# Optimization experiments

Measured on AMD Instinct MI355X. Metric: run time of the kernel, lower is better.

The kernel has to match this reference:

```python
import jax, jax.numpy as jnp
import numpy as np

D_MODEL = 1024
N_HEAD = 16
HEAD_DIM = D_MODEL // N_HEAD
B, S = 4, 2048


def setup_inputs() -> dict:
    key = jax.random.key(0)
    ks = jax.random.split(key, 11)
    s = 1.0 / np.sqrt(D_MODEL)
    return {
        "query": jax.random.normal(ks[0], (B, S, D_MODEL), jnp.float32),
        "key": jax.random.normal(ks[1], (B, S, D_MODEL), jnp.float32),
        "value": jax.random.normal(ks[2], (B, S, D_MODEL), jnp.float32),
        "Wq": jax.random.normal(ks[3], (D_MODEL, D_MODEL), jnp.float32) * s,
        "bq": jax.random.normal(ks[4], (D_MODEL,), jnp.float32) * s,
        "Wk": jax.random.normal(ks[5], (D_MODEL, D_MODEL), jnp.float32) * s,
        "bk": jax.random.normal(ks[6], (D_MODEL,), jnp.float32) * s,
        "Wv": jax.random.normal(ks[7], (D_MODEL, D_MODEL), jnp.float32) * s,
        "bv": jax.random.normal(ks[8], (D_MODEL,), jnp.float32) * s,
        "Wo": jax.random.normal(ks[9], (D_MODEL, D_MODEL), jnp.float32) * s,
        "bo": jax.random.normal(ks[10], (D_MODEL,), jnp.float32) * s,
    }


def reference(query, key, value, Wq, bq, Wk, bk, Wv, bv, Wo, bo):
    b, s, d_model = query.shape
    # projections; reshape to [b, h, s, hd]
    def proj(x, W, bias):
        return (x @ W + bias).reshape(b, s, N_HEAD, HEAD_DIM).transpose(0, 2, 1, 3)
    q = proj(query, Wq, bq)
    k = proj(key, Wk, bk)
    v = proj(value, Wv, bv)
    # NOTE: original code scales by sqrt(d_model) (bug-faithful), not sqrt(head_dim)
    scores = jnp.einsum("bhqd,bhkd->bhqk", q, k) / jnp.sqrt(jnp.float32(d_model))
    causal = jnp.tril(jnp.ones((s, s), dtype=bool))
    scores = jnp.where(causal[None, None], scores, -jnp.inf)
    p = jax.nn.softmax(scores, axis=-1)  # dropout is identity in eval
    x = jnp.einsum("bhqk,bhkd->bhqd", p, v)
    x = x.transpose(0, 2, 1, 3).reshape(b, s, d_model)
    return x @ Wo + bo
```

## Files before the change

### kernel.cpp

```cpp
#include <hip/hip_runtime.h>
#include <hip/hip_bf16.h>
#include <cstdint>
#include <cstddef>

#define D_MODEL 1024
#define N_HEAD 16
#define HEAD_DIM 64
#define BATCH 4
#define SEQ 2048
#define M_ROWS (BATCH * SEQ)

typedef __attribute__((ext_vector_type(8))) short short8v;
typedef __attribute__((ext_vector_type(4))) float f32x4;
typedef __attribute__((ext_vector_type(16))) float f32x16;

__device__ __forceinline__ unsigned short f2bf(float f) {
    union { uint32_t i; float f; } c;
    c.f = f;
    uint32_t r = c.i + 0x7FFFu + ((c.i >> 16) & 1u);
    return (unsigned short)(r >> 16);
}
__device__ __forceinline__ unsigned short trunc_bf(float f) {
    return (unsigned short)(__float_as_uint(f) >> 16);
}
__device__ __forceinline__ uint32_t pack_trunc2(float a, float b) {
    return __builtin_amdgcn_perm(__float_as_uint(b), __float_as_uint(a), 0x07060302u);
}
__device__ __forceinline__ uint32_t pack_rne2(float a, float b) {
    return (uint32_t)f2bf(a) | ((uint32_t)f2bf(b) << 16);
}

struct __align__(16) U4 { uint32_t x, y, z, w; };
struct __align__(8) U2 { uint32_t x, y; };

__device__ __forceinline__ int sw_off(int row, int gl) {
    return row * 64 + ((gl ^ (row & 7)) << 3);
}

__device__ __forceinline__ void gload16(const unsigned short *g, unsigned short *l) {
    __builtin_amdgcn_global_load_lds((const __attribute__((address_space(1))) void *)g,
                                     (__attribute__((address_space(3))) void *)l, 16, 0, 0);
}

__global__ __launch_bounds__(256)
void cvt_kernel(const float *__restrict__ src, unsigned short *__restrict__ dst)
{
    const size_t i = ((size_t)blockIdx.x * 256 + threadIdx.x) * 8;
    float4 lo = *(const float4 *)(src + i);
    float4 hi = *(const float4 *)(src + i + 4);
    U4 pk;
    pk.x = pack_trunc2(lo.x, lo.y);
    pk.y = pack_trunc2(lo.z, lo.w);
    pk.z = pack_trunc2(hi.x, hi.y);
    pk.w = pack_trunc2(hi.z, hi.w);
    *(U4 *)(dst + i) = pk;
}

__global__ __launch_bounds__(256)
void wtrans_kernel(const float *__restrict__ W, unsigned short *__restrict__ Wt)
{
    __shared__ float tile[32][33];
    const int t = threadIdx.x;
    const int tx = t & 31, ty = t >> 5;
    const int bk = blockIdx.y * 32, bn = blockIdx.x * 32;
#pragma unroll
    for (int i = 0; i < 4; i++)
        tile[ty + 8 * i][tx] = W[(size_t)(bk + ty + 8 * i) * D_MODEL + bn + tx];
    __syncthreads();
#pragma unroll
    for (int i = 0; i < 4; i++)
        Wt[(size_t)(bn + ty + 8 * i) * D_MODEL + bk + tx] = trunc_bf(tile[tx][ty + 8 * i]);
}

template <typename TA, int MODE, typename TO>
__global__ __launch_bounds__(256, 2)
void mgemm_kernel(const TA *__restrict__ A,
                  const unsigned short *__restrict__ Wt,
                  const float *__restrict__ bias,
                  TO *__restrict__ out,
                  float escale)
{
    __shared__ __align__(16) unsigned short At[2][128 * 64];
    __shared__ __align__(16) unsigned short Bt[2][128 * 64];

    const int t = threadIdx.x;
    const int wave = t >> 6;
    const int lane = t & 63;
    const int n_ = lane & 15;
    const int quad = lane >> 4;
    const int wm = wave >> 1, wn = wave & 1;
    const int m0 = blockIdx.x * 128;
    const int n0 = blockIdx.y * 128;

    f32x4 acc[4][4];
#pragma unroll
    for (int i = 0; i < 4; i++)
#pragma unroll
        for (int j = 0; j < 4; j++) acc[i][j] = (f32x4){0.f, 0.f, 0.f, 0.f};

    const int srow = t >> 3;
    const int sg = t & 7;
    const int rl = lane >> 3;
    const int gsw = (lane & 7) ^ rl;

    for (int k0 = 0; k0 < D_MODEL; k0 += 128) {
        __syncthreads();
        if constexpr (sizeof(TA) == 2) {
            const unsigned short *Ab = (const unsigned short *)A;
#pragma unroll
            for (int h = 0; h < 2; h++)
#pragma unroll
                for (int c = 0; c < 4; c++) {
                    const int rb = wave * 32 + c * 8;
                    gload16(Ab + (size_t)(m0 + rb + rl) * D_MODEL + k0 + h * 64 + (gsw << 3),
                            &At[h][rb * 64]);
                    gload16(Wt + (size_t)(n0 + rb + rl) * D_MODEL + k0 + h * 64 + (gsw << 3),
                            &Bt[h][rb * 64]);
                }
        } else {
#pragma unroll
            for (int h = 0; h < 2; h++) {
#pragma unroll
                for (int i = 0; i < 4; i++) {
                    const int r = srow + 32 * i;
                    const float *p =
                        (const float *)A + (size_t)(m0 + r) * D_MODEL + k0 + h * 64 + sg * 8;
                    float4 lo = *(const float4 *)p;
                    float4 hi = *(const float4 *)(p + 4);
                    U4 pk;
                    pk.x = pack_trunc2(lo.x, lo.y);
                    pk.y = pack_trunc2(lo.z, lo.w);
                    pk.z = pack_trunc2(hi.x, hi.y);
                    pk.w = pack_trunc2(hi.z, hi.w);
                    *(U4 *)&At[h][sw_off(r, sg)] = pk;
                }
#pragma unroll
                for (int i = 0; i < 4; i++) {
                    const int r = srow + 32 * i;
                    const unsigned short *p =
                        Wt + (size_t)(n0 + r) * D_MODEL + k0 + h * 64 + sg * 8;
                    *(U4 *)&Bt[h][sw_off(r, sg)] = *(const U4 *)p;
                }
            }
        }
        __syncthreads();

#pragma unroll
        for (int c = 0; c < 4; c++) {
            const int bk_ = c >> 1, cc = c & 1;
            short8v af[4], bf[4];
#pragma unroll
            for (int mt = 0; mt < 4; mt++)
                af[mt] = *(const short8v *)&At[bk_][sw_off(wm * 64 + mt * 16 + n_, cc * 4 + quad)];
#pragma unroll
            for (int nt = 0; nt < 4; nt++)
                bf[nt] = *(const short8v *)&Bt[bk_][sw_off(wn * 64 + nt * 16 + n_, cc * 4 + quad)];
#pragma unroll
            for (int mt = 0; mt < 4; mt++)
#pragma unroll
                for (int nt = 0; nt < 4; nt++)
                    acc[mt][nt] = __builtin_amdgcn_mfma_f32_16x16x32_bf16(
                        af[mt], bf[nt], acc[mt][nt], 0, 0, 0);
        }
    }

    float bi[4];
#pragma unroll
    for (int nt = 0; nt < 4; nt++) bi[nt] = bias[n0 + wn * 64 + nt * 16 + n_];

    if constexpr (MODE == 2) {
#pragma unroll
        for (int mt = 0; mt < 4; mt++) {
            const int m = m0 + wm * 64 + mt * 16 + quad * 4;
#pragma unroll
            for (int nt = 0; nt < 4; nt++) {
                const int col = n0 + wn * 64 + nt * 16 + n_;
                const size_t idx = ((size_t)(m >> 11) * D_MODEL + col) * SEQ + (m & 2047);
                U2 pk;
                pk.x = pack_rne2(acc[mt][nt][0] + bi[nt], acc[mt][nt][1] + bi[nt]);
                pk.y = pack_rne2(acc[mt][nt][2] + bi[nt], acc[mt][nt][3] + bi[nt]);
                *(U2 *)((unsigned short *)out + idx) = pk;
            }
        }
    } else {
#pragma unroll
        for (int mt = 0; mt < 4; mt++)
#pragma unroll
            for (int reg = 0; reg < 4; reg++) {
                const int m = m0 + wm * 64 + mt * 16 + quad * 4 + reg;
#pragma unroll
                for (int nt = 0; nt < 4; nt++) {
                    const int col = n0 + wn * 64 + nt * 16 + n_;
                    const float v = (acc[mt][nt][reg] + bi[nt]) * escale;
                    if constexpr (MODE == 1)
                        ((unsigned short *)out)[(size_t)m * D_MODEL + col] = f2bf(v);
                    else
                        ((float *)out)[(size_t)m * D_MODEL + col] = v;
                }
            }
    }
}

__global__ __launch_bounds__(256, 2)
void attn_kernel(const unsigned short *Qg,
                 const unsigned short *__restrict__ Kg,
                 const unsigned short *__restrict__ VTg,
                 unsigned short *AO)
{
    __shared__ __align__(16) unsigned short Kt[64 * 64];
    __shared__ __align__(16) unsigned short Vt[64 * 64];

    const int h = blockIdx.x;
    const int b = blockIdx.y;
    const int qpair = blockIdx.z;
    const int t = threadIdx.x;
    const int w = t >> 6;
    const int lane = t & 63;
    const int ql = lane & 31;
    const int hi = lane >> 5;

    const size_t row_base = (size_t)b * SEQ * D_MODEL + h * HEAD_DIM;
    const size_t vhead = (size_t)(b * N_HEAD + h) * HEAD_DIM * SEQ;

    const int r0 = t >> 3;
    const int g = t & 7;

#pragma unroll
    for (int pass = 0; pass < 2; ++pass) {
        const int qb = pass ? (15 - qpair) : qpair;
        const int qs0 = qb * 128 + w * 32;
        const int qseq = qs0 + ql;

        short8v qf[4];
#pragma unroll
        for (int c = 0; c < 4; c++)
            qf[c] = *(const short8v *)(Qg + row_base + (size_t)qseq * D_MODEL + c * 16 + hi * 8);

        float m_i = -INFINITY, l_i = 0.f;
        f32x16 Oacc[2];
#pragma unroll
        for (int dt = 0; dt < 2; dt++)
#pragma unroll
            for (int i = 0; i < 16; i++) Oacc[dt][i] = 0.f;

        const int kb_max = 2 * qb + 1;

        for (int kb = 0; kb <= kb_max; ++kb) {
            __syncthreads();
#pragma unroll
            for (int i = 0; i < 2; i++) {
                const int r = r0 + 32 * i;
                U4 kv = *(const U4 *)(Kg + row_base + (size_t)(kb * 64 + r) * D_MODEL + g * 8);
                *(U4 *)&Kt[sw_off(r, g)] = kv;
                U4 vv = *(const U4 *)(VTg + vhead + (size_t)r * SEQ + kb * 64 + g * 8);
                *(U4 *)&Vt[sw_off(r, g)] = vv;
            }
            __syncthreads();

            if (kb * 64 > qs0 + 31) continue;

            f32x16 st[2];
            __builtin_amdgcn_s_setprio(1);
#pragma unroll
            for (int kt = 0; kt < 2; kt++) {
#pragma unroll
                for (int i = 0; i < 16; i++) st[kt][i] = 0.f;
#pragma unroll
                for (int c = 0; c < 4; c++) {
                    short8v kf = *(const short8v *)&Kt[sw_off(kt * 32 + ql, c * 2 + hi)];
                    st[kt] = __builtin_amdgcn_mfma_f32_32x32x16_bf16(kf, qf[c], st[kt], 0, 0, 0);
                }
            }
            __builtin_amdgcn_s_setprio(0);

            if (kb * 64 + 63 > qs0) {
#pragma unroll
                for (int kt = 0; kt < 2; kt++)
#pragma unroll
                    for (int r = 0; r < 16; r++) {
                        const int kseq = kb * 64 + kt * 32 + (r & 3) + 8 * (r >> 2) + 4 * hi;
                        if (kseq > qseq) st[kt][r] = -INFINITY;
                    }
            }

            float mx = -INFINITY;
#pragma unroll
            for (int kt = 0; kt < 2; kt++)
#pragma unroll
                for (int r = 0; r < 16; r++) mx = fmaxf(mx, st[kt][r]);
            mx = fmaxf(mx, __shfl_xor(mx, 32, 64));
            const float mnew = fmaxf(m_i, mx);
            const float alpha = __builtin_amdgcn_exp2f(m_i - mnew);
            m_i = mnew;
            float rs = 0.f;
#pragma unroll
            for (int kt = 0; kt < 2; kt++)
#pragma unroll
                for (int r = 0; r < 16; r++) {
                    const float p = __builtin_amdgcn_exp2f(st[kt][r] - mnew);
                    st[kt][r] = p;
                    rs += p;
                }
            rs += __shfl_xor(rs, 32, 64);
            l_i = l_i * alpha + rs;
#pragma unroll
            for (int dt = 0; dt < 2; dt++)
#pragma unroll
                for (int r = 0; r < 16; r++) Oacc[dt][r] *= alpha;

            short8v pf[4];
#pragma unroll
            for (int tt = 0; tt < 4; tt++) {
                const int kt = tt >> 1, o = (tt & 1) * 8;
                const uint32_t A  = pack_trunc2(st[kt][o + 0], st[kt][o + 1]);
                const uint32_t A2 = pack_trunc2(st[kt][o + 2], st[kt][o + 3]);
                const uint32_t B  = pack_trunc2(st[kt][o + 4], st[kt][o + 5]);
                const uint32_t B2 = pack_trunc2(st[kt][o + 6], st[kt][o + 7]);
                const uint32_t c1 = (uint32_t)__shfl_xor((int)(hi ? A : B), 32, 64);
                const uint32_t c2 = (uint32_t)__shfl_xor((int)(hi ? A2 : B2), 32, 64);
                union { uint32_t u[4]; short8v s; } cv;
                cv.u[0] = hi ? c1 : A;
                cv.u[1] = hi ? c2 : A2;
                cv.u[2] = hi ? B : c1;
                cv.u[3] = hi ? B2 : c2;
                pf[tt] = cv.s;
            }

            __builtin_amdgcn_s_setprio(1);
#pragma unroll
            for (int dt = 0; dt < 2; dt++)
#pragma unroll
                for (int tt = 0; tt < 4; tt++) {
                    short8v vf = *(const short8v *)&Vt[sw_off(dt * 32 + ql, tt * 2 + hi)];
                    Oacc[dt] = __builtin_amdgcn_mfma_f32_32x32x16_bf16(vf, pf[tt], Oacc[dt], 0, 0, 0);
                }
            __builtin_amdgcn_s_setprio(0);
        }

        const float linv = 1.f / l_i;
        const size_t obase = row_base + (size_t)qseq * D_MODEL;
#pragma unroll
        for (int dt = 0; dt < 2; dt++)
#pragma unroll
            for (int rg = 0; rg < 4; rg++) {
                const int d0 = dt * 32 + 8 * rg + 4 * hi;
                U2 pk;
                pk.x = (uint32_t)f2bf(Oacc[dt][4 * rg + 0] * linv) |
                       ((uint32_t)f2bf(Oacc[dt][4 * rg + 1] * linv) << 16);
                pk.y = (uint32_t)f2bf(Oacc[dt][4 * rg + 2] * linv) |
                       ((uint32_t)f2bf(Oacc[dt][4 * rg + 3] * linv) << 16);
                *(U2 *)(AO + obase + d0) = pk;
            }
    }
}

extern "C" void kernel_launch(void *const *d_in, const int *in_sizes, int n_in,
                              void *d_out, int out_size, void *d_ws, size_t ws_size,
                              hipStream_t stream)
{
    const float *q  = (const float *)d_in[0];
    const float *k  = (const float *)d_in[1];
    const float *v  = (const float *)d_in[2];
    const float *Wq = (const float *)d_in[3];
    const float *bq = (const float *)d_in[4];
    const float *Wk = (const float *)d_in[5];
    const float *bk = (const float *)d_in[6];
    const float *Wv = (const float *)d_in[7];
    const float *bv = (const float *)d_in[8];
    const float *Wo = (const float *)d_in[9];
    const float *bo = (const float *)d_in[10];
    float *out = (float *)d_out;

    const size_t TENS = (size_t)M_ROWS * D_MODEL;
    const size_t WT = (size_t)D_MODEL * D_MODEL;

    unsigned short *qbuf = (unsigned short *)d_ws;
    unsigned short *kbuf = qbuf + TENS;
    unsigned short *vtbuf = kbuf + TENS;
    unsigned short *cbuf = vtbuf + TENS;
    unsigned short *wt_new = cbuf + TENS;
    unsigned short *wt_old = vtbuf + TENS;

    dim3 wgrid(32, 32);
    dim3 ggrid(M_ROWS / 128, D_MODEL / 128);
    const int cgrid = (int)(TENS / 8 / 256);

    const float qscale = 0.03125f * 1.44269504088896341f;

    const size_t need_new = (5 * TENS + WT) * sizeof(unsigned short);

    if (ws_size >= need_new) {
        unsigned short *wt = wt_new;
        wtrans_kernel<<<wgrid, 256, 0, stream>>>(Wq, wt);
        cvt_kernel<<<cgrid, 256, 0, stream>>>(q, cbuf);
        mgemm_kernel<unsigned short, 1, unsigned short><<<ggrid, 256, 0, stream>>>(cbuf, wt, bq, qbuf, qscale);
        wtrans_kernel<<<wgrid, 256, 0, stream>>>(Wk, wt);
        cvt_kernel<<<cgrid, 256, 0, stream>>>(k, cbuf);
        mgemm_kernel<unsigned short, 1, unsigned short><<<ggrid, 256, 0, stream>>>(cbuf, wt, bk, kbuf, 1.f);
        wtrans_kernel<<<wgrid, 256, 0, stream>>>(Wv, wt);
        cvt_kernel<<<cgrid, 256, 0, stream>>>(v, cbuf);
        mgemm_kernel<unsigned short, 2, unsigned short><<<ggrid, 256, 0, stream>>>(cbuf, wt, bv, vtbuf, 1.f);

        attn_kernel<<<dim3(N_HEAD, BATCH, SEQ / 256), 256, 0, stream>>>(qbuf, kbuf, vtbuf, qbuf);

        wtrans_kernel<<<wgrid, 256, 0, stream>>>(Wo, wt);
        mgemm_kernel<unsigned short, 3, float><<<ggrid, 256, 0, stream>>>(qbuf, wt, bo, out, 1.f);
    } else {
        unsigned short *wt = wt_old;
        wtrans_kernel<<<wgrid, 256, 0, stream>>>(Wq, wt);
        mgemm_kernel<float, 1, unsigned short><<<ggrid, 256, 0, stream>>>(q, wt, bq, qbuf, qscale);
        wtrans_kernel<<<wgrid, 256, 0, stream>>>(Wk, wt);
        mgemm_kernel<float, 1, unsigned short><<<ggrid, 256, 0, stream>>>(k, wt, bk, kbuf, 1.f);
        wtrans_kernel<<<wgrid, 256, 0, stream>>>(Wv, wt);
        mgemm_kernel<float, 2, unsigned short><<<ggrid, 256, 0, stream>>>(v, wt, bv, vtbuf, 1.f);

        attn_kernel<<<dim3(N_HEAD, BATCH, SEQ / 256), 256, 0, stream>>>(qbuf, kbuf, vtbuf, qbuf);

        wtrans_kernel<<<wgrid, 256, 0, stream>>>(Wo, wt);
        mgemm_kernel<unsigned short, 3, float><<<ggrid, 256, 0, stream>>>(qbuf, wt, bo, out, 1.f);
    }
}
```

Measured before the change: 321.4 us.

## Batch Q/K projections in one GEMM launch and stage 128-key blocks in attention

Adds a combined Q/K projection GEMM that runs both projections in a single launch via a z-grid dimension. It uses single-buffered LDS at higher occupancy and reuses the output buffer as scratch for converted K. The attention kernel now loads two 64-key K/V tiles per sync step, which halves the number of barrier round-trips. The trade-off is double the LDS in attention and a new GEMM variant with no double buffering, which may expose load latency.

After: 321.9 us. No clear change (+0.2%).

```diff
diff --git a/kernel.cpp b/kernel.cpp
--- a/kernel.cpp
+++ b/kernel.cpp
@@ -72,6 +72,86 @@
         Wt[(size_t)(bn + ty + 8 * i) * D_MODEL + bk + tx] = trunc_bf(tile[tx][ty + 8 * i]);
 }
 
+__global__ __launch_bounds__(256, 4)
+void qk_gemm_kernel(const unsigned short *__restrict__ cq,
+                    const unsigned short *__restrict__ ckb,
+                    const unsigned short *__restrict__ wt2,
+                    const float *__restrict__ bq, const float *__restrict__ bk,
+                    unsigned short *__restrict__ oq, unsigned short *__restrict__ ok,
+                    float qscale)
+{
+    __shared__ __align__(16) unsigned short At[128 * 64];
+    __shared__ __align__(16) unsigned short Bt[128 * 64];
+
+    const int z = blockIdx.z;
+    const unsigned short *A = z ? ckb : cq;
+    const unsigned short *Wt = wt2 + (size_t)z * D_MODEL * D_MODEL;
+    const float *bias = z ? bk : bq;
+    unsigned short *out = z ? ok : oq;
+    const float es = z ? 1.f : qscale;
+
+    const int t = threadIdx.x;
+    const int wave = t >> 6;
+    const int lane = t & 63;
+    const int n_ = lane & 15;
+    const int quad = lane >> 4;
+    const int wm = wave >> 1, wn = wave & 1;
+    const int m0 = blockIdx.x * 128;
+    const int n0 = blockIdx.y * 128;
+
+    f32x4 acc[4][4];
+#pragma unroll
+    for (int i = 0; i < 4; i++)
+#pragma unroll
+        for (int j = 0; j < 4; j++) acc[i][j] = (f32x4){0.f, 0.f, 0.f, 0.f};
+
+    const int rl = lane >> 3;
+    const int gsw = (lane & 7) ^ rl;
+
+    for (int k0 = 0; k0 < D_MODEL; k0 += 64) {
+        __syncthreads();
+#pragma unroll
+        for (int c = 0; c < 4; c++) {
+            const int rb = wave * 32 + c * 8;
+            gload16(A + (size_t)(m0 + rb + rl) * D_MODEL + k0 + (gsw << 3), &At[rb * 64]);
+            gload16(Wt + (size_t)(n0 + rb + rl) * D_MODEL + k0 + (gsw << 3), &Bt[rb * 64]);
+        }
+        __syncthreads();
+
+#pragma unroll
+        for (int c = 0; c < 2; c++) {
+            short8v af[4], bf[4];
+#pragma unroll
+            for (int mt = 0; mt < 4; mt++)
+                af[mt] = *(const short8v *)&At[sw_off(wm * 64 + mt * 16 + n_, c * 4 + quad)];
+#pragma unroll
+            for (int nt = 0; nt < 4; nt++)
+                bf[nt] = *(const short8v *)&Bt[sw_off(wn * 64 + nt * 16 + n_, c * 4 + quad)];
+#pragma unroll
+            for (int mt = 0; mt < 4; mt++)
+#pragma unroll
+                for (int nt = 0; nt < 4; nt++)
+                    acc[mt][nt] = __builtin_amdgcn_mfma_f32_16x16x32_bf16(
+                        af[mt], bf[nt], acc[mt][nt], 0, 0, 0);
+        }
+    }
+
+    float bi[4];
+#pragma unroll
+    for (int nt = 0; nt < 4; nt++) bi[nt] = bias[n0 + wn * 64 + nt * 16 + n_];
+#pragma unroll
+    for (int mt = 0; mt < 4; mt++)
+#pragma unroll
+        for (int reg = 0; reg < 4; reg++) {
+            const int m = m0 + wm * 64 + mt * 16 + quad * 4 + reg;
+#pragma unroll
+            for (int nt = 0; nt < 4; nt++) {
+                const int col = n0 + wn * 64 + nt * 16 + n_;
+                out[(size_t)m * D_MODEL + col] = f2bf((acc[mt][nt][reg] + bi[nt]) * es);
+            }
+        }
+}
+
 template <typename TA, int MODE, typename TO>
 __global__ __launch_bounds__(256, 2)
 void mgemm_kernel(const TA *__restrict__ A,
@@ -207,8 +287,8 @@
                  const unsigned short *__restrict__ VTg,
                  unsigned short *AO)
 {
-    __shared__ __align__(16) unsigned short Kt[64 * 64];
-    __shared__ __align__(16) unsigned short Vt[64 * 64];
+    __shared__ __align__(16) unsigned short Kt[2][64 * 64];
+    __shared__ __align__(16) unsigned short Vt[2][64 * 64];
 
     const int h = blockIdx.x;
     const int b = blockIdx.y;
@@ -243,98 +323,106 @@
 #pragma unroll
             for (int i = 0; i < 16; i++) Oacc[dt][i] = 0.f;
 
-        const int kb_max = 2 * qb + 1;
-
-        for (int kb = 0; kb <= kb_max; ++kb) {
+        const int nst = qb + 1;
+
+        for (int s = 0; s <= nst - 1; ++s) {
             __syncthreads();
 #pragma unroll
-            for (int i = 0; i < 2; i++) {
-                const int r = r0 + 32 * i;
-                U4 kv = *(const U4 *)(Kg + row_base + (size_t)(kb * 64 + r) * D_MODEL + g * 8);
-                *(U4 *)&Kt[sw_off(r, g)] = kv;
-                U4 vv = *(const U4 *)(VTg + vhead + (size_t)r * SEQ + kb * 64 + g * 8);
-                *(U4 *)&Vt[sw_off(r, g)] = vv;
+            for (int bk2 = 0; bk2 < 2; bk2++)
+#pragma unroll
+                for (int i = 0; i < 2; i++) {
+                    const int r = r0 + 32 * i;
+                    U4 kv = *(const U4 *)(Kg + row_base +
+                                          (size_t)(s * 128 + bk2 * 64 + r) * D_MODEL + g * 8);
+                    *(U4 *)&Kt[bk2][sw_off(r, g)] = kv;
+                    U4 vv = *(const U4 *)(VTg + vhead + (size_t)r * SEQ + s * 128 + bk2 * 64 + g * 8);
+                    *(U4 *)&Vt[bk2][sw_off(r, g)] = vv;
+                }
+            __syncthreads();
+
+#pragma unroll
+            for (int h2 = 0; h2 < 2; h2++) {
+                const int kv0 = s * 128 + h2 * 64;
+                if (kv0 > qs0 + 31) continue;
+
+                f32x16 st[2];
+                __builtin_amdgcn_s_setprio(1);
+#pragma unroll
+                for (int kt = 0; kt < 2; kt++) {
+#pragma unroll
+                    for (int i = 0; i < 16; i++) st[kt][i] = 0.f;
+#pragma unroll
+                    for (int c = 0; c < 4; c++) {
+                        short8v kf = *(const short8v *)&Kt[h2][sw_off(kt * 32 + ql, c * 2 + hi)];
+                        st[kt] = __builtin_amdgcn_mfma_f32_32x32x16_bf16(kf, qf[c], st[kt], 0, 0, 0);
+                    }
+                }
+                __builtin_amdgcn_s_setprio(0);
+
+                if (kv0 + 63 > qs0) {
+#pragma unroll
+                    for (int kt = 0; kt < 2; kt++)
+#pragma unroll
+                        for (int r = 0; r < 16; r++) {
+                            const int kseq = kv0 + kt * 32 + (r & 3) + 8 * (r >> 2) + 4 * hi;
+                            if (kseq > qseq) st[kt][r] = -INFINITY;
+                        }
+                }
+
+                float mx = -INFINITY;
+#pragma unroll
+                for (int kt = 0; kt < 2; kt++)
+#pragma unroll
+                    for (int r = 0; r < 16; r++) mx = fmaxf(mx, st[kt][r]);
+                mx = fmaxf(mx, __shfl_xor(mx, 32, 64));
+                const float mnew = fmaxf(m_i, mx);
+                const float alpha = __builtin_amdgcn_exp2f(m_i - mnew);
+                m_i = mnew;
+                float rs = 0.f;
+#pragma unroll
+                for (int kt = 0; kt < 2; kt++)
+#pragma unroll
+                    for (int r = 0; r < 16; r++) {
+                        const float p = __builtin_amdgcn_exp2f(st[kt][r] - mnew);
+                        st[kt][r] = p;
+                        rs += p;
+                    }
+                rs += __shfl_xor(rs, 32, 64);
+                l_i = l_i * alpha + rs;
+#pragma unroll
+                for (int dt = 0; dt < 2; dt++)
+#pragma unroll
+                    for (int r = 0; r < 16; r++) Oacc[dt][r] *= alpha;
+
+                short8v pf[4];
+#pragma unroll
+                for (int tt = 0; tt < 4; tt++) {
+                    const int kt = tt >> 1, o = (tt & 1) * 8;
+                    const uint32_t A  = pack_trunc2(st[kt][o + 0], st[kt][o + 1]);
+                    const uint32_t A2 = pack_trunc2(st[kt][o + 2], st[kt][o + 3]);
+                    const uint32_t B  = pack_trunc2(st[kt][o + 4], st[kt][o + 5]);
+                    const uint32_t B2 = pack_trunc2(st[kt][o + 6], st[kt][o + 7]);
+                    const uint32_t c1 = (uint32_t)__shfl_xor((int)(hi ? A : B), 32, 64);
+                    const uint32_t c2 = (uint32_t)__shfl_xor((int)(hi ? A2 : B2), 32, 64);
+                    union { uint32_t u[4]; short8v s; } cv;
+                    cv.u[0] = hi ? c1 : A;
+                    cv.u[1] = hi ? c2 : A2;
+                    cv.u[2] = hi ? B : c1;
+                    cv.u[3] = hi ? B2 : c2;
+                    pf[tt] = cv.s;
+                }
+
+                __builtin_amdgcn_s_setprio(1);
+#pragma unroll
+                for (int dt = 0; dt < 2; dt++)
+#pragma unroll
+                    for (int tt = 0; tt < 4; tt++) {
+                        short8v vf = *(const short8v *)&Vt[h2][sw_off(dt * 32 + ql, tt * 2 + hi)];
+                        Oacc[dt] =
+                            __builtin_amdgcn_mfma_f32_32x32x16_bf16(vf, pf[tt], Oacc[dt], 0, 0, 0);
+                    }
+                __builtin_amdgcn_s_setprio(0);
             }
-            __syncthreads();
-
-            if (kb * 64 > qs0 + 31) continue;
-
-            f32x16 st[2];
-            __builtin_amdgcn_s_setprio(1);
-#pragma unroll
-            for (int kt = 0; kt < 2; kt++) {
-#pragma unroll
-                for (int i = 0; i < 16; i++) st[kt][i] = 0.f;
-#pragma unroll
-                for (int c = 0; c < 4; c++) {
-                    short8v kf = *(const short8v *)&Kt[sw_off(kt * 32 + ql, c * 2 + hi)];
-                    st[kt] = __builtin_amdgcn_mfma_f32_32x32x16_bf16(kf, qf[c], st[kt], 0, 0, 0);
-                }
-            }
-            __builtin_amdgcn_s_setprio(0);
-
-            if (kb * 64 + 63 > qs0) {
-#pragma unroll
-                for (int kt = 0; kt < 2; kt++)
-#pragma unroll
-                    for (int r = 0; r < 16; r++) {
-                        const int kseq = kb * 64 + kt * 32 + (r & 3) + 8 * (r >> 2) + 4 * hi;
-                        if (kseq > qseq) st[kt][r] = -INFINITY;
-                    }
-            }
-
-            float mx = -INFINITY;
-#pragma unroll
-            for (int kt = 0; kt < 2; kt++)
-#pragma unroll
-                for (int r = 0; r < 16; r++) mx = fmaxf(mx, st[kt][r]);
-            mx = fmaxf(mx, __shfl_xor(mx, 32, 64));
-            const float mnew = fmaxf(m_i, mx);
-            const float alpha = __builtin_amdgcn_exp2f(m_i - mnew);
-            m_i = mnew;
-            float rs = 0.f;
-#pragma unroll
-            for (int kt = 0; kt < 2; kt++)
-#pragma unroll
-                for (int r = 0; r < 16; r++) {
-                    const float p = __builtin_amdgcn_exp2f(st[kt][r] - mnew);
-                    st[kt][r] = p;
-                    rs += p;
-                }
-            rs += __shfl_xor(rs, 32, 64);
-            l_i = l_i * alpha + rs;
-#pragma unroll
-            for (int dt = 0; dt < 2; dt++)
-#pragma unroll
-                for (int r = 0; r < 16; r++) Oacc[dt][r] *= alpha;
-
-            short8v pf[4];
-#pragma unroll
-            for (int tt = 0; tt < 4; tt++) {
-                const int kt = tt >> 1, o = (tt & 1) * 8;
-                const uint32_t A  = pack_trunc2(st[kt][o + 0], st[kt][o + 1]);
-                const uint32_t A2 = pack_trunc2(st[kt][o + 2], st[kt][o + 3]);
-                const uint32_t B  = pack_trunc2(st[kt][o + 4], st[kt][o + 5]);
-                const uint32_t B2 = pack_trunc2(st[kt][o + 6], st[kt][o + 7]);
-                const uint32_t c1 = (uint32_t)__shfl_xor((int)(hi ? A : B), 32, 64);
-                const uint32_t c2 = (uint32_t)__shfl_xor((int)(hi ? A2 : B2), 32, 64);
-                union { uint32_t u[4]; short8v s; } cv;
-                cv.u[0] = hi ? c1 : A;
-                cv.u[1] = hi ? c2 : A2;
-                cv.u[2] = hi ? B : c1;
-                cv.u[3] = hi ? B2 : c2;
-                pf[tt] = cv.s;
-            }
-
-            __builtin_amdgcn_s_setprio(1);
-#pragma unroll
-            for (int dt = 0; dt < 2; dt++)
-#pragma unroll
-                for (int tt = 0; tt < 4; tt++) {
-                    short8v vf = *(const short8v *)&Vt[sw_off(dt * 32 + ql, tt * 2 + hi)];
-                    Oacc[dt] = __builtin_amdgcn_mfma_f32_32x32x16_bf16(vf, pf[tt], Oacc[dt], 0, 0, 0);
-                }
-            __builtin_amdgcn_s_setprio(0);
         }
 
         const float linv = 1.f / l_i;
@@ -374,39 +462,43 @@
     const size_t TENS = (size_t)M_ROWS * D_MODEL;
     const size_t WT = (size_t)D_MODEL * D_MODEL;
 
-    unsigned short *qbuf = (unsigned short *)d_ws;
-    unsigned short *kbuf = qbuf + TENS;
-    unsigned short *vtbuf = kbuf + TENS;
-    unsigned short *cbuf = vtbuf + TENS;
-    unsigned short *wt_new = cbuf + TENS;
-    unsigned short *wt_old = vtbuf + TENS;
-
     dim3 wgrid(32, 32);
     dim3 ggrid(M_ROWS / 128, D_MODEL / 128);
     const int cgrid = (int)(TENS / 8 / 256);
-
     const float qscale = 0.03125f * 1.44269504088896341f;
 
-    const size_t need_new = (5 * TENS + WT) * sizeof(unsigned short);
-
-    if (ws_size >= need_new) {
-        unsigned short *wt = wt_new;
-        wtrans_kernel<<<wgrid, 256, 0, stream>>>(Wq, wt);
-        cvt_kernel<<<cgrid, 256, 0, stream>>>(q, cbuf);
-        mgemm_kernel<unsigned short, 1, unsigned short><<<ggrid, 256, 0, stream>>>(cbuf, wt, bq, qbuf, qscale);
-        wtrans_kernel<<<wgrid, 256, 0, stream>>>(Wk, wt);
-        cvt_kernel<<<cgrid, 256, 0, stream>>>(k, cbuf);
-        mgemm_kernel<unsigned short, 1, unsigned short><<<ggrid, 256, 0, stream>>>(cbuf, wt, bk, kbuf, 1.f);
-        wtrans_kernel<<<wgrid, 256, 0, stream>>>(Wv, wt);
-        cvt_kernel<<<cgrid, 256, 0, stream>>>(v, cbuf);
-        mgemm_kernel<unsigned short, 2, unsigned short><<<ggrid, 256, 0, stream>>>(cbuf, wt, bv, vtbuf, 1.f);
+    const size_t need_new = (4 * TENS + 2 * WT) * sizeof(unsigned short);
+
+    if (ws_size >= need_new && (size_t)out_size >= TENS * sizeof(unsigned short)) {
+        unsigned short *qbuf = (unsigned short *)d_ws;
+        unsigned short *kbuf = qbuf + TENS;
+        unsigned short *vtbuf = kbuf + TENS;
+        unsigned short *cq = vtbuf + TENS;
+        unsigned short *wt2 = cq + TENS;
+        unsigned short *ck = (unsigned short *)d_out;
+
+        wtrans_kernel<<<wgrid, 256, 0, stream>>>(Wq, wt2);
+        wtrans_kernel<<<wgrid, 256, 0, stream>>>(Wk, wt2 + WT);
+        cvt_kernel<<<cgrid, 256, 0, stream>>>(q, cq);
+        cvt_kernel<<<cgrid, 256, 0, stream>>>(k, ck);
+        qk_gemm_kernel<<<dim3(M_ROWS / 128, D_MODEL / 128, 2), 256, 0, stream>>>(
+            cq, ck, wt2, bq, bk, qbuf, kbuf, qscale);
+
+        wtrans_kernel<<<wgrid, 256, 0, stream>>>(Wv, wt2);
+        cvt_kernel<<<cgrid, 256, 0, stream>>>(v, cq);
+        mgemm_kernel<unsigned short, 2, unsigned short><<<ggrid, 256, 0, stream>>>(
+            cq, wt2, bv, vtbuf, 1.f);
 
         attn_kernel<<<dim3(N_HEAD, BATCH, SEQ / 256), 256, 0, stream>>>(qbuf, kbuf, vtbuf, qbuf);
 
-        wtrans_kernel<<<wgrid, 256, 0, stream>>>(Wo, wt);
-        mgemm_kernel<unsigned short, 3, float><<<ggrid, 256, 0, stream>>>(qbuf, wt, bo, out, 1.f);
+        wtrans_kernel<<<wgrid, 256, 0, stream>>>(Wo, wt2);
+        mgemm_kernel<unsigned short, 3, float><<<ggrid, 256, 0, stream>>>(qbuf, wt2, bo, out, 1.f);
     } else {
-        unsigned short *wt = wt_old;
+        unsigned short *qbuf = (unsigned short *)d_ws;
+        unsigned short *kbuf = qbuf + TENS;
+        unsigned short *vtbuf = kbuf + TENS;
+        unsigned short *wt = vtbuf + TENS;
+
         wtrans_kernel<<<wgrid, 256, 0, stream>>>(Wq, wt);
         mgemm_kernel<float, 1, unsigned short><<<ggrid, 256, 0, stream>>>(q, wt, bq, qbuf, qscale);
         wtrans_kernel<<<wgrid, 256, 0, stream>>>(Wk, wt);
```
